# Kernel tuning notes

Hardware: AMD Instinct MI355X
Metric: run time of the kernel (lower is better)

The kernel has to match this reference:

```python
import jax, jax.numpy as jnp
import numpy as np

G = 8            # n_group
C = 256          # input_dim / channels
N_MEM = C // G   # 32
ALPHA = 0.4      # w_alpha
EPS = 1e-5
SLOPE = 0.01     # LeakyReLU negative slope


def _lrelu(x):
    return jnp.where(x >= 0, x, SLOPE * x)


def _mlp(x, ws, bs):
    # torch nn.Linear convention: y = x @ W.T + b; lrelu on all but last layer
    n = len(ws)
    for i in range(n):
        x = x @ ws[i].T + bs[i]
        if i < n - 1:
            x = _lrelu(x)
    return x


def _wct(c_A, s_B, mask, ct_ws, ct_bs, mu_ws, mu_bs):
    B, Cc, H, W = c_A.shape
    n_mem = Cc // G
    # style -> per-group coloring matrices  (Get.coloring, vectorized over groups)
    s_CT = _mlp(s_B.reshape(B * G, n_mem), ct_ws, ct_bs).reshape(B, G, n_mem, n_mem)
    D = jnp.sqrt(jnp.sum(s_CT ** 2, axis=2, keepdims=True))        # [B,G,1,n_mem]
    U = s_CT / D                                                    # column-normalized
    UDU = jnp.einsum('bgij,bgkj->bgik', s_CT, U)                    # [B,G,n_mem,n_mem]
    # torch.cat(U_arr, dim=0) is group-major: index g*B+b
    eigen_s = jnp.transpose(U, (1, 0, 2, 3)).reshape(G * B, n_mem, n_mem)
    X = jnp.tile(UDU.reshape(B, Cc, n_mem), (1, 1, G)) * mask       # [B,C,C]
    s_mu = _mlp(s_B, mu_ws, mu_bs)[:, :, None, None]                # [B,C,1,1]
    # per-group covariance of mean-centered content
    c_g = jnp.transpose(c_A, (1, 0, 2, 3)).reshape(G, n_mem, B * H * W)
    c_g = c_g - jnp.mean(c_g, axis=2, keepdims=True)
    cov_c = jnp.einsum('gin,gjn->gij', c_g, c_g) / (B * H * W - 1) \
        + EPS * jnp.eye(n_mem, dtype=c_A.dtype)
    # centered content, reinterpreted as [B, C, H*W] (matches torch view/permute)
    whitend = jnp.transpose(c_g.reshape(Cc, B, H * W), (1, 0, 2))
    colored = jnp.einsum('bcd,bdn->bcn', X, whitend).reshape(B, Cc, H, W)
    out = ALPHA * (colored + s_mu) + (1.0 - ALPHA) * c_A
    return out, cov_c, eigen_s


def setup_inputs():
    key = jax.random.key(0)
    ks = jax.random.split(key, 16)
    B, H, W = 4, 128, 128
    c_A = jax.random.normal(ks[0], (B, C, H, W), dtype=jnp.float32)
    s_B = jax.random.normal(ks[1], (B, C), dtype=jnp.float32)
    # block-diagonal group mask [1, C, C]
    m = np.zeros((C, C), dtype=np.float32)
    for g in range(G):
        m[g * N_MEM:(g + 1) * N_MEM, g * N_MEM:(g + 1) * N_MEM] = 1.0
    mask = jnp.asarray(m)[None]

    def lin(k, o, i):
        return jax.random.normal(k, (o, i), dtype=jnp.float32) * (1.0 / np.sqrt(i))

    inp = {'c_A': c_A, 's_B': s_B, 'mask': mask}
    dims_ct = [(256, 32), (256, 256), (256, 256), (256, 256), (1024, 256)]
    for j, (o, i) in enumerate(dims_ct):
        inp['ct_w%d' % j] = lin(ks[2 + j], o, i)
        inp['ct_b%d' % j] = jnp.zeros((o,), dtype=jnp.float32)
    dims_mu = [(256, 256), (256, 256), (256, 256)]
    for j, (o, i) in enumerate(dims_mu):
        inp['mu_w%d' % j] = lin(ks[8 + j], o, i)
        inp['mu_b%d' % j] = jnp.zeros((o,), dtype=jnp.float32)
    return inp


def reference(c_A, s_B, mask, ct_w0, ct_b0, ct_w1, ct_b1, ct_w2, ct_b2,
              ct_w3, ct_b3, ct_w4, ct_b4, mu_w0, mu_b0, mu_w1, mu_b1,
              mu_w2, mu_b2):
    ct_ws = (ct_w0, ct_w1, ct_w2, ct_w3, ct_w4)
    ct_bs = (ct_b0, ct_b1, ct_b2, ct_b3, ct_b4)
    mu_ws = (mu_w0, mu_w1, mu_w2)
    mu_bs = (mu_b0, mu_b1, mu_b2)
    return _wct(c_A, s_B, mask, ct_ws, ct_bs, mu_ws, mu_bs)
```

## Files before the change

kernel.cpp:

```cpp
#include <hip/hip_runtime.h>
#include <hip/hip_bf16.h>

typedef __bf16 bf16x8 __attribute__((ext_vector_type(8)));
typedef float  f32x16 __attribute__((ext_vector_type(16)));

#define ALPHA_W 0.4f

#define OUT_MAIN 16777216
#define OUT_COV  (OUT_MAIN)
#define OUT_EIG  (OUT_MAIN + 8192)

#define WS_SX   0
#define WS_SXY  256
#define WS_CTA  8448
#define WS_CTB  41216
#define WS_MUA  73984
#define WS_MUB  75008
#define WS_SMU  76032
#define WS_M    77056
#define WS_T    109824

struct LinJob {
    const float* X;
    const float* Wt;
    const float* Bi;
    float* Y;
    int in, out, act;
};

__global__ __launch_bounds__(256) void lin_kernel(LinJob a, LinJob b, int nb0) {
    LinJob j = (blockIdx.x < (unsigned)nb0) ? a : b;
    int bid  = (blockIdx.x < (unsigned)nb0) ? blockIdx.x : blockIdx.x - nb0;
    int obpr = j.out >> 8;
    int row  = bid / obpr;
    int oc   = bid % obpr;
    __shared__ float xs[256];
    int t = threadIdx.x;
    if (t < j.in) xs[t] = j.X[row * j.in + t];
    __syncthreads();
    int o = oc * 256 + t;
    const float* wr = j.Wt + (size_t)o * j.in;
    float acc = 0.f;
    for (int i = 0; i < j.in; i += 4) {
        float4 wv = *(const float4*)(wr + i);
        acc = fmaf(wv.x, xs[i + 0], acc);
        acc = fmaf(wv.y, xs[i + 1], acc);
        acc = fmaf(wv.z, xs[i + 2], acc);
        acc = fmaf(wv.w, xs[i + 3], acc);
    }
    acc += j.Bi[o];
    if (j.act) acc = acc >= 0.f ? acc : 0.01f * acc;
    j.Y[(size_t)row * j.out + o] = acc;
}

__global__ __launch_bounds__(256) void gram_kernel(const float* __restrict__ cA,
                                                   float* __restrict__ SX,
                                                   float* __restrict__ SXY) {
    int bid = blockIdx.x;
    int g = bid >> 5, slice = bid & 31;
    int tid = threadIdx.x;
    int w = tid >> 6, l = tid & 63;
    int col = l & 31, kq = l >> 5;
    int nbase = slice * 2048 + w * 512;
    int b = nbase >> 14;
    int hw0 = nbase & 16383;
    const float* base = cA + (((size_t)(b * 256 + g * 32 + col)) << 14) + hw0 + kq * 8;

    f32x16 acc;
    #pragma unroll
    for (int r = 0; r < 16; r++) acc[r] = 0.f;
    float s = 0.f;
    for (int it = 0; it < 32; ++it) {
        float4 f0 = *(const float4*)(base + it * 16);
        float4 f1 = *(const float4*)(base + it * 16 + 4);
        s += f0.x + f0.y + f0.z + f0.w + f1.x + f1.y + f1.z + f1.w;
        bf16x8 v;
        v[0] = (__bf16)f0.x; v[1] = (__bf16)f0.y; v[2] = (__bf16)f0.z; v[3] = (__bf16)f0.w;
        v[4] = (__bf16)f1.x; v[5] = (__bf16)f1.y; v[6] = (__bf16)f1.z; v[7] = (__bf16)f1.w;
        acc = __builtin_amdgcn_mfma_f32_32x32x16_bf16(v, v, acc, 0, 0, 0);
    }
    __shared__ float red[4][1024];
    __shared__ float sxr[4][64];
    sxr[w][l] = s;
    #pragma unroll
    for (int r = 0; r < 16; r++) {
        int i = (r & 3) + 8 * (r >> 2) + 4 * kq;
        red[w][i * 32 + col] = acc[r];
    }
    __syncthreads();
    for (int e = tid; e < 1024; e += 256) {
        float v = red[0][e] + red[1][e] + red[2][e] + red[3][e];
        atomicAdd(&SXY[g * 1024 + e], v);
    }
    if (tid < 32) {
        float v = 0.f;
        #pragma unroll
        for (int ww = 0; ww < 4; ww++) v += sxr[ww][tid] + sxr[ww][tid + 32];
        atomicAdd(&SX[g * 32 + tid], v);
    }
}

__global__ __launch_bounds__(256) void small_kernel(const float* __restrict__ CT,
                                                    const float* __restrict__ SMU,
                                                    const float* __restrict__ SX,
                                                    const float* __restrict__ SXY,
                                                    float* __restrict__ M,
                                                    float* __restrict__ T,
                                                    float* __restrict__ out) {
    int bid = blockIdx.x;
    int t = threadIdx.x;
    if (bid < 32) {
        int b = bid >> 3, g = bid & 7;
        __shared__ float sct[32 * 33], uu[32 * 33], ud[32 * 33], dinv[32];
        const float* src = CT + (size_t)(b * 8 + g) * 1024;
        for (int e = t; e < 1024; e += 256) sct[(e >> 5) * 33 + (e & 31)] = src[e];
        __syncthreads();
        if (t < 32) {
            float s = 0.f;
            for (int i = 0; i < 32; i++) { float v = sct[i * 33 + t]; s = fmaf(v, v, s); }
            dinv[t] = 1.0f / sqrtf(s);
        }
        __syncthreads();
        float* eig = out + OUT_EIG + (size_t)(g * 4 + b) * 1024;
        for (int e = t; e < 1024; e += 256) {
            int i = e >> 5, jj = e & 31;
            float u = sct[i * 33 + jj] * dinv[jj];
            uu[i * 33 + jj] = u;
            eig[e] = u;
        }
        __syncthreads();
        float* Mo = M + (size_t)(b * 8 + g) * 1024;
        for (int e = t; e < 1024; e += 256) {
            int i = e >> 5, k = e & 31;
            float s = 0.f;
            for (int jv = 0; jv < 32; jv++) s = fmaf(sct[i * 33 + jv], uu[k * 33 + jv], s);
            ud[i * 33 + k] = s;
            Mo[e] = ALPHA_W * s + (i == k ? (1.0f - ALPHA_W) : 0.0f);
        }
        __syncthreads();
        if (t < 32) {
            float s = 0.f;
            for (int k = 0; k < 32; k++)
                s = fmaf(ud[t * 33 + k], SX[g * 32 + k] * (1.0f / 65536.0f), s);
            T[(b * 8 + g) * 32 + t] = ALPHA_W * (SMU[b * 256 + g * 32 + t] - s);
        }
    } else {
        int g = bid - 32;
        float* cov = out + OUT_COV + (size_t)g * 1024;
        for (int e = t; e < 1024; e += 256) {
            int i = e >> 5, jj = e & 31;
            float mi = SX[g * 32 + i] * (1.0f / 65536.0f);
            float mj = SX[g * 32 + jj] * (1.0f / 65536.0f);
            float v = (SXY[g * 1024 + e] - 65536.0f * mi * mj) * (1.0f / 65535.0f);
            if (i == jj) v += 1e-5f;
            cov[e] = v;
        }
    }
}

__global__ __launch_bounds__(256) void color_kernel(const float* __restrict__ cA,
                                                    const float* __restrict__ M,
                                                    const float* __restrict__ T,
                                                    float* __restrict__ out) {
    int bid = blockIdx.x;
    int bg = bid >> 5, chunk = bid & 31;
    int b = bg >> 3, g = bg & 7;
    int tid = threadIdx.x;
    int n = tid & 63, ih = tid >> 6;
    __shared__ float Ml[1024];
    __shared__ float tl[32];
    __shared__ float xs[32 * 64];
    for (int e = tid; e < 1024; e += 256) Ml[e] = M[(size_t)bg * 1024 + e];
    if (tid < 32) tl[tid] = T[bg * 32 + tid];
    size_t cbase = (((size_t)(b * 256 + g * 32)) << 14) + chunk * 512;
    int srow = tid >> 3, scol = (tid & 7) * 8;
    for (int tile = 0; tile < 8; ++tile) {
        const float* src = cA + cbase + (size_t)srow * 16384 + tile * 64 + scol;
        float4 u0 = *(const float4*)src;
        float4 u1 = *(const float4*)(src + 4);
        __syncthreads();
        float* xd = &xs[srow * 64 + scol];
        xd[0] = u0.x; xd[1] = u0.y; xd[2] = u0.z; xd[3] = u0.w;
        xd[4] = u1.x; xd[5] = u1.y; xd[6] = u1.z; xd[7] = u1.w;
        __syncthreads();
        float acc[8];
        #pragma unroll
        for (int i = 0; i < 8; i++) acc[i] = tl[ih * 8 + i];
        for (int k = 0; k < 32; k++) {
            float xv = xs[k * 64 + n];
            #pragma unroll
            for (int i = 0; i < 8; i++) acc[i] = fmaf(Ml[(ih * 8 + i) * 32 + k], xv, acc[i]);
        }
        float* dst = out + (((size_t)(b * 256 + g * 32 + ih * 8)) << 14)
                     + chunk * 512 + tile * 64 + n;
        #pragma unroll
        for (int i = 0; i < 8; i++) dst[(size_t)i << 14] = acc[i];
    }
}

extern "C" void kernel_launch(void* const* d_in, const int* in_sizes, int n_in,
                              void* d_out, int out_size, void* d_ws, size_t ws_size,
                              hipStream_t stream) {
    (void)in_sizes; (void)n_in; (void)out_size; (void)ws_size;
    const float* cA = (const float*)d_in[0];
    const float* sB = (const float*)d_in[1];
    const float* ctw[5] = {(const float*)d_in[3], (const float*)d_in[5], (const float*)d_in[7],
                           (const float*)d_in[9], (const float*)d_in[11]};
    const float* ctb[5] = {(const float*)d_in[4], (const float*)d_in[6], (const float*)d_in[8],
                           (const float*)d_in[10], (const float*)d_in[12]};
    const float* muw[3] = {(const float*)d_in[13], (const float*)d_in[15], (const float*)d_in[17]};
    const float* mub[3] = {(const float*)d_in[14], (const float*)d_in[16], (const float*)d_in[18]};
    float* W = (float*)d_ws;
    float* out = (float*)d_out;

    hipMemsetAsync(W + WS_SX, 0, (256 + 8192) * sizeof(float), stream);

    gram_kernel<<<256, 256, 0, stream>>>(cA, W + WS_SX, W + WS_SXY);

    LinJob a, b;
    a = {sB, ctw[0], ctb[0], W + WS_CTA, 32, 256, 1};
    b = {sB, muw[0], mub[0], W + WS_MUA, 256, 256, 1};
    lin_kernel<<<36, 256, 0, stream>>>(a, b, 32);
    a = {W + WS_CTA, ctw[1], ctb[1], W + WS_CTB, 256, 256, 1};
    b = {W + WS_MUA, muw[1], mub[1], W + WS_MUB, 256, 256, 1};
    lin_kernel<<<36, 256, 0, stream>>>(a, b, 32);
    a = {W + WS_CTB, ctw[2], ctb[2], W + WS_CTA, 256, 256, 1};
    b = {W + WS_MUB, muw[2], mub[2], W + WS_SMU, 256, 256, 0};
    lin_kernel<<<36, 256, 0, stream>>>(a, b, 32);
    a = {W + WS_CTA, ctw[3], ctb[3], W + WS_CTB, 256, 256, 1};
    lin_kernel<<<32, 256, 0, stream>>>(a, a, 32);
    a = {W + WS_CTB, ctw[4], ctb[4], W + WS_CTA, 256, 1024, 0};
    lin_kernel<<<128, 256, 0, stream>>>(a, a, 128);

    small_kernel<<<40, 256, 0, stream>>>(W + WS_CTA, W + WS_SMU, W + WS_SX, W + WS_SXY,
                                         W + WS_M, W + WS_T, out);

    color_kernel<<<1024, 256, 0, stream>>>(cA, W + WS_M, W + WS_T, out);
}
```

Measured before the change: 230.8 us.

## Fuse MLP chain into finalize kernel and replace gram atomics with partial sums

The five ct and three mu linear-layer launches and the small finalize kernel are merged into one mlp_finalize kernel. Each of its 32 blocks recomputes the full MLP for its (b,g) in shared memory. The gram kernel now writes per-block partial sums instead of doing atomicAdds, so the memset is gone and the finalize kernel reduces the partials. The color kernel double-buffers its shared tile with vector stores, dropping one barrier per tile. This removes about six launches and their serialization, but repeats the MLP weight reads across 32 blocks (8x redundant) and runs the serial MLP on only 40 blocks.

```diff
diff --git a/kernel.cpp b/kernel.cpp
--- a/kernel.cpp
+++ b/kernel.cpp
@@ -5,57 +5,25 @@
 typedef float  f32x16 __attribute__((ext_vector_type(16)));
 
 #define ALPHA_W 0.4f
+#define NTOT 65536.0f
 
 #define OUT_MAIN 16777216
 #define OUT_COV  (OUT_MAIN)
 #define OUT_EIG  (OUT_MAIN + 8192)
 
-#define WS_SX   0
-#define WS_SXY  256
-#define WS_CTA  8448
-#define WS_CTB  41216
-#define WS_MUA  73984
-#define WS_MUB  75008
-#define WS_SMU  76032
-#define WS_M    77056
-#define WS_T    109824
-
-struct LinJob {
-    const float* X;
-    const float* Wt;
-    const float* Bi;
-    float* Y;
-    int in, out, act;
+#define WS_PSXY 0
+#define WS_PSX  262144
+#define WS_M    270336
+#define WS_T    303104
+
+struct Ptrs {
+    const float* ctw[5]; const float* ctb[5];
+    const float* muw[3]; const float* mub[3];
 };
 
-__global__ __launch_bounds__(256) void lin_kernel(LinJob a, LinJob b, int nb0) {
-    LinJob j = (blockIdx.x < (unsigned)nb0) ? a : b;
-    int bid  = (blockIdx.x < (unsigned)nb0) ? blockIdx.x : blockIdx.x - nb0;
-    int obpr = j.out >> 8;
-    int row  = bid / obpr;
-    int oc   = bid % obpr;
-    __shared__ float xs[256];
-    int t = threadIdx.x;
-    if (t < j.in) xs[t] = j.X[row * j.in + t];
-    __syncthreads();
-    int o = oc * 256 + t;
-    const float* wr = j.Wt + (size_t)o * j.in;
-    float acc = 0.f;
-    for (int i = 0; i < j.in; i += 4) {
-        float4 wv = *(const float4*)(wr + i);
-        acc = fmaf(wv.x, xs[i + 0], acc);
-        acc = fmaf(wv.y, xs[i + 1], acc);
-        acc = fmaf(wv.z, xs[i + 2], acc);
-        acc = fmaf(wv.w, xs[i + 3], acc);
-    }
-    acc += j.Bi[o];
-    if (j.act) acc = acc >= 0.f ? acc : 0.01f * acc;
-    j.Y[(size_t)row * j.out + o] = acc;
-}
-
 __global__ __launch_bounds__(256) void gram_kernel(const float* __restrict__ cA,
-                                                   float* __restrict__ SX,
-                                                   float* __restrict__ SXY) {
+                                                   float* __restrict__ pSXY,
+                                                   float* __restrict__ pSX) {
     int bid = blockIdx.x;
     int g = bid >> 5, slice = bid & 31;
     int tid = threadIdx.x;
@@ -69,11 +37,12 @@
     f32x16 acc;
     #pragma unroll
     for (int r = 0; r < 16; r++) acc[r] = 0.f;
-    float s = 0.f;
+    float s0 = 0.f, s1 = 0.f;
     for (int it = 0; it < 32; ++it) {
         float4 f0 = *(const float4*)(base + it * 16);
         float4 f1 = *(const float4*)(base + it * 16 + 4);
-        s += f0.x + f0.y + f0.z + f0.w + f1.x + f1.y + f1.z + f1.w;
+        s0 += (f0.x + f0.y) + (f0.z + f0.w);
+        s1 += (f1.x + f1.y) + (f1.z + f1.w);
         bf16x8 v;
         v[0] = (__bf16)f0.x; v[1] = (__bf16)f0.y; v[2] = (__bf16)f0.z; v[3] = (__bf16)f0.w;
         v[4] = (__bf16)f1.x; v[5] = (__bf16)f1.y; v[6] = (__bf16)f1.z; v[7] = (__bf16)f1.w;
@@ -81,7 +50,7 @@
     }
     __shared__ float red[4][1024];
     __shared__ float sxr[4][64];
-    sxr[w][l] = s;
+    sxr[w][l] = s0 + s1;
     #pragma unroll
     for (int r = 0; r < 16; r++) {
         int i = (r & 3) + 8 * (r >> 2) + 4 * kq;
@@ -89,21 +58,41 @@
     }
     __syncthreads();
     for (int e = tid; e < 1024; e += 256) {
-        float v = red[0][e] + red[1][e] + red[2][e] + red[3][e];
-        atomicAdd(&SXY[g * 1024 + e], v);
+        pSXY[(size_t)bid * 1024 + e] = red[0][e] + red[1][e] + red[2][e] + red[3][e];
     }
     if (tid < 32) {
         float v = 0.f;
         #pragma unroll
         for (int ww = 0; ww < 4; ww++) v += sxr[ww][tid] + sxr[ww][tid + 32];
-        atomicAdd(&SX[g * 32 + tid], v);
-    }
-}
-
-__global__ __launch_bounds__(256) void small_kernel(const float* __restrict__ CT,
-                                                    const float* __restrict__ SMU,
-                                                    const float* __restrict__ SX,
-                                                    const float* __restrict__ SXY,
+        pSX[bid * 32 + tid] = v;
+    }
+}
+
+__device__ inline float dot256(const float* __restrict__ w, const float* __restrict__ x) {
+    float a0 = 0.f, a1 = 0.f, a2 = 0.f, a3 = 0.f;
+    for (int i = 0; i < 256; i += 16) {
+        float4 w0 = *(const float4*)(w + i);
+        float4 w1 = *(const float4*)(w + i + 4);
+        float4 w2 = *(const float4*)(w + i + 8);
+        float4 w3 = *(const float4*)(w + i + 12);
+        a0 = fmaf(w0.x, x[i + 0], a0);  a0 = fmaf(w0.y, x[i + 1], a0);
+        a0 = fmaf(w0.z, x[i + 2], a0);  a0 = fmaf(w0.w, x[i + 3], a0);
+        a1 = fmaf(w1.x, x[i + 4], a1);  a1 = fmaf(w1.y, x[i + 5], a1);
+        a1 = fmaf(w1.z, x[i + 6], a1);  a1 = fmaf(w1.w, x[i + 7], a1);
+        a2 = fmaf(w2.x, x[i + 8], a2);  a2 = fmaf(w2.y, x[i + 9], a2);
+        a2 = fmaf(w2.z, x[i + 10], a2); a2 = fmaf(w2.w, x[i + 11], a2);
+        a3 = fmaf(w3.x, x[i + 12], a3); a3 = fmaf(w3.y, x[i + 13], a3);
+        a3 = fmaf(w3.z, x[i + 14], a3); a3 = fmaf(w3.w, x[i + 15], a3);
+    }
+    return (a0 + a1) + (a2 + a3);
+}
+
+__device__ inline float lrelu(float x) { return x >= 0.f ? x : 0.01f * x; }
+
+__global__ __launch_bounds__(256) void mlp_finalize(const float* __restrict__ sB,
+                                                    Ptrs p,
+                                                    const float* __restrict__ pSXY,
+                                                    const float* __restrict__ pSX,
                                                     float* __restrict__ M,
                                                     float* __restrict__ T,
                                                     float* __restrict__ out) {
@@ -111,10 +100,45 @@
     int t = threadIdx.x;
     if (bid < 32) {
         int b = bid >> 3, g = bid & 7;
-        __shared__ float sct[32 * 33], uu[32 * 33], ud[32 * 33], dinv[32];
-        const float* src = CT + (size_t)(b * 8 + g) * 1024;
-        for (int e = t; e < 1024; e += 256) sct[(e >> 5) * 33 + (e & 31)] = src[e];
-        __syncthreads();
+        __shared__ float ha[256], hb[256];
+        __shared__ float sct[32 * 33], uu[32 * 33], ud[32 * 33];
+        __shared__ float dinv[32], sxg[32];
+        if (t < 32) {
+            ha[t] = sB[b * 256 + g * 32 + t];
+            float s = 0.f;
+            for (int sl = 0; sl < 32; sl++) s += pSX[(g * 32 + sl) * 32 + t];
+            sxg[t] = s * (1.0f / NTOT);
+        }
+        __syncthreads();
+        {
+            const float* wr = p.ctw[0] + t * 32;
+            float a0 = 0.f, a1 = 0.f;
+            #pragma unroll
+            for (int i = 0; i < 32; i += 8) {
+                float4 w0 = *(const float4*)(wr + i);
+                float4 w1 = *(const float4*)(wr + i + 4);
+                a0 = fmaf(w0.x, ha[i + 0], a0); a0 = fmaf(w0.y, ha[i + 1], a0);
+                a0 = fmaf(w0.z, ha[i + 2], a0); a0 = fmaf(w0.w, ha[i + 3], a0);
+                a1 = fmaf(w1.x, ha[i + 4], a1); a1 = fmaf(w1.y, ha[i + 5], a1);
+                a1 = fmaf(w1.z, ha[i + 6], a1); a1 = fmaf(w1.w, ha[i + 7], a1);
+            }
+            hb[t] = lrelu(a0 + a1 + p.ctb[0][t]);
+        }
+        __syncthreads();
+        ha[t] = lrelu(dot256(p.ctw[1] + t * 256, hb) + p.ctb[1][t]);  __syncthreads();
+        hb[t] = lrelu(dot256(p.ctw[2] + t * 256, ha) + p.ctb[2][t]);  __syncthreads();
+        ha[t] = lrelu(dot256(p.ctw[3] + t * 256, hb) + p.ctb[3][t]);  __syncthreads();
+        #pragma unroll
+        for (int q = 0; q < 4; q++) {
+            int o = t + 256 * q;
+            float v = dot256(p.ctw[4] + (size_t)o * 256, ha) + p.ctb[4][o];
+            sct[(o >> 5) * 33 + (o & 31)] = v;
+        }
+        __syncthreads();
+        ha[t] = sB[b * 256 + t];                                      __syncthreads();
+        hb[t] = lrelu(dot256(p.muw[0] + t * 256, ha) + p.mub[0][t]);  __syncthreads();
+        ha[t] = lrelu(dot256(p.muw[1] + t * 256, hb) + p.mub[1][t]);  __syncthreads();
+        hb[t] = dot256(p.muw[2] + t * 256, ha) + p.mub[2][t];
         if (t < 32) {
             float s = 0.f;
             for (int i = 0; i < 32; i++) { float v = sct[i * 33 + t]; s = fmaf(v, v, s); }
@@ -129,7 +153,7 @@
             eig[e] = u;
         }
         __syncthreads();
-        float* Mo = M + (size_t)(b * 8 + g) * 1024;
+        float* Mo = M + (size_t)bid * 1024;
         for (int e = t; e < 1024; e += 256) {
             int i = e >> 5, k = e & 31;
             float s = 0.f;
@@ -140,18 +164,24 @@
         __syncthreads();
         if (t < 32) {
             float s = 0.f;
-            for (int k = 0; k < 32; k++)
-                s = fmaf(ud[t * 33 + k], SX[g * 32 + k] * (1.0f / 65536.0f), s);
-            T[(b * 8 + g) * 32 + t] = ALPHA_W * (SMU[b * 256 + g * 32 + t] - s);
+            for (int k = 0; k < 32; k++) s = fmaf(ud[t * 33 + k], sxg[k], s);
+            T[bid * 32 + t] = ALPHA_W * (hb[g * 32 + t] - s);
         }
     } else {
         int g = bid - 32;
+        __shared__ float sxg[32];
+        if (t < 32) {
+            float s = 0.f;
+            for (int sl = 0; sl < 32; sl++) s += pSX[(g * 32 + sl) * 32 + t];
+            sxg[t] = s * (1.0f / NTOT);
+        }
+        __syncthreads();
         float* cov = out + OUT_COV + (size_t)g * 1024;
         for (int e = t; e < 1024; e += 256) {
+            float s = 0.f;
+            for (int sl = 0; sl < 32; sl++) s += pSXY[(size_t)(g * 32 + sl) * 1024 + e];
             int i = e >> 5, jj = e & 31;
-            float mi = SX[g * 32 + i] * (1.0f / 65536.0f);
-            float mj = SX[g * 32 + jj] * (1.0f / 65536.0f);
-            float v = (SXY[g * 1024 + e] - 65536.0f * mi * mj) * (1.0f / 65535.0f);
+            float v = (s - NTOT * sxg[i] * sxg[jj]) * (1.0f / (NTOT - 1.0f));
             if (i == jj) v += 1e-5f;
             cov[e] = v;
         }
@@ -169,30 +199,30 @@
     int n = tid & 63, ih = tid >> 6;
     __shared__ float Ml[1024];
     __shared__ float tl[32];
-    __shared__ float xs[32 * 64];
+    __shared__ float xs[2][2048];
     for (int e = tid; e < 1024; e += 256) Ml[e] = M[(size_t)bg * 1024 + e];
     if (tid < 32) tl[tid] = T[bg * 32 + tid];
     size_t cbase = (((size_t)(b * 256 + g * 32)) << 14) + chunk * 512;
     int srow = tid >> 3, scol = (tid & 7) * 8;
+    size_t obase = (((size_t)(b * 256 + g * 32 + ih * 8)) << 14) + chunk * 512 + n;
     for (int tile = 0; tile < 8; ++tile) {
         const float* src = cA + cbase + (size_t)srow * 16384 + tile * 64 + scol;
         float4 u0 = *(const float4*)src;
         float4 u1 = *(const float4*)(src + 4);
-        __syncthreads();
-        float* xd = &xs[srow * 64 + scol];
-        xd[0] = u0.x; xd[1] = u0.y; xd[2] = u0.z; xd[3] = u0.w;
-        xd[4] = u1.x; xd[5] = u1.y; xd[6] = u1.z; xd[7] = u1.w;
-        __syncthreads();
+        float* xd = &xs[tile & 1][srow * 64 + scol];
+        *(float4*)xd = u0;
+        *(float4*)(xd + 4) = u1;
+        __syncthreads();
+        const float* xb = xs[tile & 1];
         float acc[8];
         #pragma unroll
         for (int i = 0; i < 8; i++) acc[i] = tl[ih * 8 + i];
         for (int k = 0; k < 32; k++) {
-            float xv = xs[k * 64 + n];
+            float xv = xb[k * 64 + n];
             #pragma unroll
             for (int i = 0; i < 8; i++) acc[i] = fmaf(Ml[(ih * 8 + i) * 32 + k], xv, acc[i]);
         }
-        float* dst = out + (((size_t)(b * 256 + g * 32 + ih * 8)) << 14)
-                     + chunk * 512 + tile * 64 + n;
+        float* dst = out + obase + tile * 64;
         #pragma unroll
         for (int i = 0; i < 8; i++) dst[(size_t)i << 14] = acc[i];
     }
@@ -204,36 +234,20 @@
     (void)in_sizes; (void)n_in; (void)out_size; (void)ws_size;
     const float* cA = (const float*)d_in[0];
     const float* sB = (const float*)d_in[1];
-    const float* ctw[5] = {(const float*)d_in[3], (const float*)d_in[5], (const float*)d_in[7],
-                           (const float*)d_in[9], (const float*)d_in[11]};
-    const float* ctb[5] = {(const float*)d_in[4], (const float*)d_in[6], (const float*)d_in[8],
-                           (const float*)d_in[10], (const float*)d_in[12]};
-    const float* muw[3] = {(const float*)d_in[13], (const float*)d_in[15], (const float*)d_in[17]};
-    const float* mub[3] = {(const float*)d_in[14], (const float*)d_in[16], (const float*)d_in[18]};
+    Ptrs p;
+    p.ctw[0] = (const float*)d_in[3];  p.ctb[0] = (const float*)d_in[4];
+    p.ctw[1] = (const float*)d_in[5];  p.ctb[1] = (const float*)d_in[6];
+    p.ctw[2] = (const float*)d_in[7];  p.ctb[2] = (const float*)d_in[8];
+    p.ctw[3] = (const float*)d_in[9];  p.ctb[3] = (const float*)d_in[10];
+    p.ctw[4] = (const float*)d_in[11]; p.ctb[4] = (const float*)d_in[12];
+    p.muw[0] = (const float*)d_in[13]; p.mub[0] = (const float*)d_in[14];
+    p.muw[1] = (const float*)d_in[15]; p.mub[1] = (const float*)d_in[16];
+    p.muw[2] = (const float*)d_in[17]; p.mub[2] = (const float*)d_in[18];
     float* W = (float*)d_ws;
     float* out = (float*)d_out;
 
-    hipMemsetAsync(W + WS_SX, 0, (256 + 8192) * sizeof(float), stream);
-
-    gram_kernel<<<256, 256, 0, stream>>>(cA, W + WS_SX, W + WS_SXY);
-
-    LinJob a, b;
-    a = {sB, ctw[0], ctb[0], W + WS_CTA, 32, 256, 1};
-    b = {sB, muw[0], mub[0], W + WS_MUA, 256, 256, 1};
-    lin_kernel<<<36, 256, 0, stream>>>(a, b, 32);
-    a = {W + WS_CTA, ctw[1], ctb[1], W + WS_CTB, 256, 256, 1};
-    b = {W + WS_MUA, muw[1], mub[1], W + WS_MUB, 256, 256, 1};
-    lin_kernel<<<36, 256, 0, stream>>>(a, b, 32);
-    a = {W + WS_CTB, ctw[2], ctb[2], W + WS_CTA, 256, 256, 1};
-    b = {W + WS_MUB, muw[2], mub[2], W + WS_SMU, 256, 256, 0};
-    lin_kernel<<<36, 256, 0, stream>>>(a, b, 32);
-    a = {W + WS_CTA, ctw[3], ctb[3], W + WS_CTB, 256, 256, 1};
-    lin_kernel<<<32, 256, 0, stream>>>(a, a, 32);
-    a = {W + WS_CTB, ctw[4], ctb[4], W + WS_CTA, 256, 1024, 0};
-    lin_kernel<<<128, 256, 0, stream>>>(a, a, 128);
-
-    small_kernel<<<40, 256, 0, stream>>>(W + WS_CTA, W + WS_SMU, W + WS_SX, W + WS_SXY,
+    gram_kernel<<<256, 256, 0, stream>>>(cA, W + WS_PSXY, W + WS_PSX);
+    mlp_finalize<<<40, 256, 0, stream>>>(sB, p, W + WS_PSXY, W + WS_PSX,
                                          W + WS_M, W + WS_T, out);
-
     color_kernel<<<1024, 256, 0, stream>>>(cA, W + WS_M, W + WS_T, out);
 }
```

Measured after the change: 283.7 us. 1.23x slower.
